# Kernel optimization log

Measured on AMD Instinct MI355X. Metric: run time of the kernel, lower is better.

## Reference

```python
import jax, jax.numpy as jnp
import numpy as np

B, S, H, NH = 2, 2048, 1024, 16
HD = H // NH  # 64
CLIP = 2.5          # clip_init_val; SymQuantizer clamps to [-CLIP, CLIP]
QMAX = 127.0        # 2**(input_bits-1) - 1 for 8-bit symmetric


def sym_quant(x):
    """BiT SymQuantizer, layerwise=True: clamp, layerwise max-abs scale,
    round-to-nearest (scale detached, as in torch .detach())."""
    xc = jnp.clip(x, -CLIP, CLIP)
    m = jax.lax.stop_gradient(jnp.max(jnp.abs(xc)))
    s = QMAX / m
    return jnp.round(xc * s) / s


def setup_inputs() -> dict:
    key = jax.random.key(0)
    ks = jax.random.split(key, 4)
    return {
        "hidden_states": jax.random.normal(ks[0], (B, S, H), jnp.float32),
        "attention_mask": jnp.zeros((B, 1, 1, S), jnp.float32),  # additive mask
        "Wq": jax.random.normal(ks[1], (H, H), jnp.float32) * 0.02,
        "bq": jnp.zeros((H,), jnp.float32),
        "Wk": jax.random.normal(ks[2], (H, H), jnp.float32) * 0.02,
        "bk": jnp.zeros((H,), jnp.float32),
        "Wv": jax.random.normal(ks[3], (H, H), jnp.float32) * 0.02,
        "bv": jnp.zeros((H,), jnp.float32),
        "move_q": jnp.zeros((H,), jnp.float32),
        "move_k": jnp.zeros((H,), jnp.float32),
        "move_v": jnp.zeros((H,), jnp.float32),
    }


def reference(hidden_states, attention_mask, Wq, bq, Wk, bk, Wv, bv,
              move_q, move_k, move_v):
    # QuantizeLinear: quantize input (same quant for all three projections)
    # and quantize weights, then F.linear + bias.
    xq = sym_quant(hidden_states)                       # [B,S,H]
    q = xq @ sym_quant(Wq).T + bq                       # [B,S,H]
    k = xq @ sym_quant(Wk).T + bk
    v = xq @ sym_quant(Wv).T + bv
    # NOTE (bug-faithful): original computes move_q/k/v(mixed_*) but then
    # re-derives query/key/value from mixed_* — LearnableBias has no effect.

    def heads(t):  # [B,S,H] -> [B,NH,S,HD]
        return t.reshape(B, S, NH, HD).transpose(0, 2, 1, 3)

    ql = sym_quant(heads(q))
    kl = sym_quant(heads(k))
    vl = sym_quant(heads(v))

    scores = jnp.einsum('bhqd,bhkd->bhqk', ql, kl) / np.float32(np.sqrt(HD))
    scores = scores + attention_mask                    # [B,NH,S,S]
    probs = jax.nn.softmax(scores, axis=-1)
    # dropout p=0.0 (eval) -> identity; quantize attention probs
    probs = sym_quant(probs)
    ctx = jnp.einsum('bhqk,bhkd->bhqd', probs, vl)      # [B,NH,S,HD]
    ctx = ctx.transpose(0, 2, 1, 3).reshape(B, S, H)
    return ctx, scores
```

## Files before the change

kernel.cpp:

```cpp
#include <hip/hip_runtime.h>
#include <stdint.h>

typedef int i32x4 __attribute__((ext_vector_type(4)));

constexpr int Bb = 2, Ss = 2048, Hh = 1024, NHn = 16;
constexpr int Mm = Bb * Ss;
constexpr int BH = Bb * NHn;
constexpr float CLIPV = 2.5f;

constexpr size_t X8_OFF   = 256;
constexpr size_t W8Q_OFF  = X8_OFF  + (size_t)Mm * Hh;
constexpr size_t W8K_OFF  = W8Q_OFF + (size_t)Hh * Hh;
constexpr size_t W8V_OFF  = W8K_OFF + (size_t)Hh * Hh;
constexpr size_t Q8_OFF   = W8V_OFF + (size_t)Hh * Hh;
constexpr size_t K8_OFF   = Q8_OFF  + (size_t)Mm * Hh;
constexpr size_t V8_OFF   = K8_OFF  + (size_t)Mm * Hh;
constexpr size_t V8T_OFF  = V8_OFF  + (size_t)Mm * Hh;
constexpr size_t RMAX_OFF = V8T_OFF + (size_t)Mm * Hh;
constexpr size_t RSUM_OFF = RMAX_OFF + (size_t)BH * Ss * 4;

__device__ __forceinline__ i32x4 zero4() {
  i32x4 z; z[0] = 0; z[1] = 0; z[2] = 0; z[3] = 0; return z;
}

__global__ void k_init(float* scal) {
  if (threadIdx.x < 7) scal[threadIdx.x] = 0.f;
  if (threadIdx.x == 7) ((unsigned int*)scal)[7] = 0x7f800000u;
}

__global__ __launch_bounds__(256) void k_absmax(
    const float* __restrict__ hs, const float* __restrict__ wq,
    const float* __restrict__ wk, const float* __restrict__ wv,
    float* __restrict__ scal) {
  int b = blockIdx.x;
  const float* src; int sidx, boff;
  if (b < 256)      { src = hs; sidx = 0; boff = b; }
  else if (b < 320) { src = wq; sidx = 1; boff = b - 256; }
  else if (b < 384) { src = wk; sidx = 2; boff = b - 320; }
  else              { src = wv; sidx = 3; boff = b - 384; }
  const float4* p = (const float4*)src + (size_t)boff * 4096 + threadIdx.x;
  float m = 0.f;
#pragma unroll
  for (int i = 0; i < 16; ++i) {
    float4 v = p[i * 256];
    m = fmaxf(m, fmaxf(fmaxf(fabsf(v.x), fabsf(v.y)), fmaxf(fabsf(v.z), fabsf(v.w))));
  }
#pragma unroll
  for (int off = 32; off; off >>= 1) m = fmaxf(m, __shfl_xor(m, off));
  __shared__ float red[4];
  if ((threadIdx.x & 63) == 0) red[threadIdx.x >> 6] = m;
  __syncthreads();
  if (threadIdx.x == 0) {
    m = fmaxf(fmaxf(red[0], red[1]), fmaxf(red[2], red[3]));
    atomicMax((unsigned int*)scal + sidx, __float_as_uint(m));
  }
}

__global__ __launch_bounds__(256) void k_quant_in(
    const float* __restrict__ hs, const float* __restrict__ wq,
    const float* __restrict__ wk, const float* __restrict__ wv,
    const float* __restrict__ scal, char* __restrict__ ws) {
  int b = blockIdx.x;
  const float* src; int sidx, boff; unsigned int* dst;
  if (b < 256)      { src = hs; sidx = 0; boff = b;       dst = (unsigned int*)(ws + X8_OFF); }
  else if (b < 320) { src = wq; sidx = 1; boff = b - 256; dst = (unsigned int*)(ws + W8Q_OFF); }
  else if (b < 384) { src = wk; sidx = 2; boff = b - 320; dst = (unsigned int*)(ws + W8K_OFF); }
  else              { src = wv; sidx = 3; boff = b - 384; dst = (unsigned int*)(ws + W8V_OFF); }
  float s = 127.f / fminf(scal[sidx], CLIPV);
  size_t base = (size_t)boff * 4096 + threadIdx.x;
  const float4* p = (const float4*)src + base;
  dst += base;
#pragma unroll
  for (int i = 0; i < 16; ++i) {
    float4 v = p[i * 256];
    int a0 = __float2int_rn(fminf(fmaxf(v.x, -CLIPV), CLIPV) * s);
    int a1 = __float2int_rn(fminf(fmaxf(v.y, -CLIPV), CLIPV) * s);
    int a2 = __float2int_rn(fminf(fmaxf(v.z, -CLIPV), CLIPV) * s);
    int a3 = __float2int_rn(fminf(fmaxf(v.w, -CLIPV), CLIPV) * s);
    dst[i * 256] = (a0 & 255) | ((a1 & 255) << 8) | ((a2 & 255) << 16) | ((a3 & 255) << 24);
  }
}

__global__ __launch_bounds__(256) void k_qkv_gemm(
    char* __restrict__ ws, float* __restrict__ qkvf,
    const float* __restrict__ bq, const float* __restrict__ bk,
    const float* __restrict__ bv, const float* __restrict__ scal) {
  int wsel = blockIdx.z;
  const char* a8 = ws + X8_OFF;
  const char* b8 = ws + (wsel == 0 ? W8Q_OFF : wsel == 1 ? W8K_OFF : W8V_OFF);
  const float* bias = wsel == 0 ? bq : wsel == 1 ? bk : bv;
  float* outp = qkvf + (size_t)wsel * Mm * Hh;
  float scaleAB = (fminf(scal[0], CLIPV) / 127.f) * (fminf(scal[1 + wsel], CLIPV) / 127.f);

  __shared__ __align__(16) char lA[64][80];
  __shared__ __align__(16) char lB[64][80];
  int t = threadIdx.x;
  int lane = t & 63, w = t >> 6, c = lane & 15, g = lane >> 4;
  int i0 = blockIdx.y * 64;
  int n0 = blockIdx.x * 64;
  int strow = t >> 2, sto = t & 3;
  int stoff = (sto ^ (strow & 3)) * 16;

  i32x4 acc[4];
#pragma unroll
  for (int nt = 0; nt < 4; ++nt) acc[nt] = zero4();

  for (int kc = 0; kc < 16; ++kc) {
    i32x4 va = *(const i32x4*)(a8 + (size_t)(i0 + strow) * 1024 + kc * 64 + sto * 16);
    i32x4 vb = *(const i32x4*)(b8 + (size_t)(n0 + strow) * 1024 + kc * 64 + sto * 16);
    __syncthreads();
    *(i32x4*)&lA[strow][stoff] = va;
    *(i32x4*)&lB[strow][stoff] = vb;
    __syncthreads();
    i32x4 af = *(const i32x4*)&lA[w * 16 + c][(g ^ (c & 3)) * 16];
#pragma unroll
    for (int nt = 0; nt < 4; ++nt) {
      i32x4 bf = *(const i32x4*)&lB[nt * 16 + c][(g ^ (c & 3)) * 16];
      acc[nt] = __builtin_amdgcn_mfma_i32_16x16x64_i8(af, bf, acc[nt], 0, 0, 0);
    }
  }
  float amax = 0.f;
#pragma unroll
  for (int nt = 0; nt < 4; ++nt) {
    int n = n0 + nt * 16 + c;
    float bvv = bias[n];
#pragma unroll
    for (int r = 0; r < 4; ++r) {
      int i = i0 + w * 16 + g * 4 + r;
      float val = fmaf((float)acc[nt][r], scaleAB, bvv);
      outp[(size_t)i * 1024 + n] = val;
      amax = fmaxf(amax, fabsf(val));
    }
  }
#pragma unroll
  for (int off = 32; off; off >>= 1) amax = fmaxf(amax, __shfl_xor(amax, off));
  if (lane == 0) atomicMax((unsigned int*)scal + 4 + wsel, __float_as_uint(amax));
}

__global__ __launch_bounds__(256) void k_quant_qkv(
    char* __restrict__ ws, const float* __restrict__ qkvf,
    const float* __restrict__ scal) {
  int b = blockIdx.x;
  int wsel = b >> 8, boff = b & 255;
  const float* src = qkvf + (size_t)wsel * Mm * Hh;
  unsigned int* dst = (unsigned int*)(ws + (wsel == 0 ? Q8_OFF : wsel == 1 ? K8_OFF : V8_OFF));
  float s = 127.f / fminf(scal[4 + wsel], CLIPV);
  size_t base = (size_t)boff * 4096 + threadIdx.x;
  const float4* p = (const float4*)src + base;
  dst += base;
#pragma unroll
  for (int i = 0; i < 16; ++i) {
    float4 v = p[i * 256];
    int a0 = __float2int_rn(fminf(fmaxf(v.x, -CLIPV), CLIPV) * s);
    int a1 = __float2int_rn(fminf(fmaxf(v.y, -CLIPV), CLIPV) * s);
    int a2 = __float2int_rn(fminf(fmaxf(v.z, -CLIPV), CLIPV) * s);
    int a3 = __float2int_rn(fminf(fmaxf(v.w, -CLIPV), CLIPV) * s);
    dst[i * 256] = (a0 & 255) | ((a1 & 255) << 8) | ((a2 & 255) << 16) | ((a3 & 255) << 24);
  }
}

__global__ __launch_bounds__(256) void k_scores(
    const char* __restrict__ ws, const float* __restrict__ mask,
    float* __restrict__ scores, float* __restrict__ rmax,
    float* __restrict__ rsum, const float* __restrict__ scal) {
  const char* q8 = ws + Q8_OFF;
  const char* k8 = ws + K8_OFF;
  int bh = blockIdx.y, b = bh >> 4;
  int h = bh & 15;
  int i0 = blockIdx.x * 64;
  int t = threadIdx.x, lane = t & 63, w = t >> 6, c = lane & 15, g = lane >> 4;
  float scale8 = (fminf(scal[4], CLIPV) / 127.f) * (fminf(scal[5], CLIPV) / 127.f) * 0.125f;

  __shared__ __align__(16) char lK[128][80];

  int irow = i0 + w * 16 + c;
  i32x4 qf = *(const i32x4*)(q8 + (size_t)(b * 2048 + irow) * 1024 + h * 64 + g * 16);
  const float* maskb = mask + b * 2048;
  float* srow_base = scores + ((size_t)bh * 2048 + irow) * 2048;

  float m = -INFINITY, l = 0.f;
  int strow = t >> 2, sto = t & 3;
  int stoff = (sto ^ (strow & 3)) * 16;

  for (int jc = 0; jc < 2048; jc += 128) {
    i32x4 v0 = *(const i32x4*)(k8 + (size_t)(b * 2048 + jc + strow) * 1024 + h * 64 + sto * 16);
    i32x4 v1 = *(const i32x4*)(k8 + (size_t)(b * 2048 + jc + 64 + strow) * 1024 + h * 64 + sto * 16);
    __syncthreads();
    *(i32x4*)&lK[strow][stoff] = v0;
    *(i32x4*)&lK[64 + strow][stoff] = v1;
    __syncthreads();
#pragma unroll
    for (int jt = 0; jt < 8; ++jt) {
      i32x4 kf = *(const i32x4*)&lK[jt * 16 + c][(g ^ (c & 3)) * 16];
      i32x4 d = __builtin_amdgcn_mfma_i32_16x16x64_i8(kf, qf, zero4(), 0, 0, 0);
      int jbase = jc + jt * 16 + g * 4;
      float4 mv = *(const float4*)(maskb + jbase);
      float s0 = fmaf((float)d[0], scale8, mv.x);
      float s1 = fmaf((float)d[1], scale8, mv.y);
      float s2 = fmaf((float)d[2], scale8, mv.z);
      float s3 = fmaf((float)d[3], scale8, mv.w);
      float tmax = fmaxf(fmaxf(s0, s1), fmaxf(s2, s3));
      float mn = fmaxf(m, tmax);
      l = fmaf(l, __expf(m - mn),
               __expf(s0 - mn) + __expf(s1 - mn) + __expf(s2 - mn) + __expf(s3 - mn));
      m = mn;
      float4 outv; outv.x = s0; outv.y = s1; outv.z = s2; outv.w = s3;
      *(float4*)(srow_base + jbase) = outv;
    }
  }
#pragma unroll
  for (int off = 16; off <= 32; off <<= 1) {
    float mo = __shfl_xor(m, off);
    float lo = __shfl_xor(l, off);
    float mn = fmaxf(m, mo);
    l = l * __expf(m - mn) + lo * __expf(mo - mn);
    m = mn;
  }
  if (g == 0) {
    rmax[(size_t)bh * 2048 + irow] = m;
    rsum[(size_t)bh * 2048 + irow] = l;
  }
  float lmin = l;
#pragma unroll
  for (int off = 1; off <= 8; off <<= 1) lmin = fminf(lmin, __shfl_xor(lmin, off));
  if (lane == 0) atomicMin((unsigned int*)scal + 7, __float_as_uint(lmin));
}

__global__ __launch_bounds__(256) void k_vtrans(char* __restrict__ ws) {
  const char* v8 = ws + V8_OFF;
  char* v8t = ws + V8T_OFF;
  int bh = blockIdx.y, b = bh >> 4, h = bh & 15;
  int jc = blockIdx.x * 64;
  __shared__ __align__(16) char tile[64][80];
  int t = threadIdx.x;
  int j = t >> 2, o = t & 3;
  i32x4 v = *(const i32x4*)(v8 + (size_t)(b * 2048 + jc + j) * 1024 + h * 64 + o * 16);
  *(i32x4*)&tile[j][o * 16] = v;
  __syncthreads();
  int d = t >> 2, seg = t & 3;
  int od[4] = {0, 0, 0, 0};
#pragma unroll
  for (int jj = 0; jj < 16; ++jj)
    od[jj >> 2] |= (int)(unsigned char)tile[seg * 16 + jj][d] << ((jj & 3) * 8);
  i32x4 ov; ov[0] = od[0]; ov[1] = od[1]; ov[2] = od[2]; ov[3] = od[3];
  *(i32x4*)(v8t + ((size_t)bh * 64 + d) * 2048 + jc + seg * 16) = ov;
}

__global__ __launch_bounds__(256) void k_pv(
    char* __restrict__ ws, const float* __restrict__ mask,
    float* __restrict__ ctx, const float* __restrict__ scal) {
  const char* q8 = ws + Q8_OFF;
  const char* k8 = ws + K8_OFF;
  const char* v8t = ws + V8T_OFF;
  const float* rmax = (const float*)(ws + RMAX_OFF);
  const float* rsum = (const float*)(ws + RSUM_OFF);
  int bh = blockIdx.y, b = bh >> 4, h = bh & 15;
  int i0 = blockIdx.x * 64;
  int t = threadIdx.x, lane = t & 63, w = t >> 6, c = lane & 15, g = lane >> 4;
  float scale8 = (fminf(scal[4], CLIPV) / 127.f) * (fminf(scal[5], CLIPV) / 127.f) * 0.125f;
  float min_l = __uint_as_float(((const unsigned int*)scal)[7]);
  float s_p = 127.f * min_l;
  float s_v = 127.f / fminf(scal[6], CLIPV);
  float oscale = 1.f / (s_p * s_v);

  __shared__ __align__(16) char lK[64][80];
  __shared__ __align__(16) int pl[4][16][20];

  int irow = i0 + w * 16 + c;
  i32x4 qf = *(const i32x4*)(q8 + (size_t)(b * 2048 + irow) * 1024 + h * 64 + g * 16);
  float m_i = rmax[(size_t)bh * 2048 + irow];
  float coef = s_p / rsum[(size_t)bh * 2048 + irow];
  const float* maskb = mask + b * 2048;

  i32x4 acc[4];
#pragma unroll
  for (int vt = 0; vt < 4; ++vt) acc[vt] = zero4();

  int strow = t >> 2, sto = t & 3;
  int stoff = (sto ^ (strow & 3)) * 16;

  for (int jc = 0; jc < 2048; jc += 64) {
    i32x4 kv = *(const i32x4*)(k8 + (size_t)(b * 2048 + jc + strow) * 1024 + h * 64 + sto * 16);
    __syncthreads();
    *(i32x4*)&lK[strow][stoff] = kv;
    __syncthreads();
#pragma unroll
    for (int jt = 0; jt < 4; ++jt) {
      i32x4 kf = *(const i32x4*)&lK[jt * 16 + c][(g ^ (c & 3)) * 16];
      i32x4 d = __builtin_amdgcn_mfma_i32_16x16x64_i8(kf, qf, zero4(), 0, 0, 0);
      int jbase = jc + jt * 16 + g * 4;
      float4 mv = *(const float4*)(maskb + jbase);
      float s0 = fmaf((float)d[0], scale8, mv.x);
      float s1 = fmaf((float)d[1], scale8, mv.y);
      float s2 = fmaf((float)d[2], scale8, mv.z);
      float s3 = fmaf((float)d[3], scale8, mv.w);
      int p0 = __float2int_rn(__expf(s0 - m_i) * coef);
      int p1 = __float2int_rn(__expf(s1 - m_i) * coef);
      int p2 = __float2int_rn(__expf(s2 - m_i) * coef);
      int p3 = __float2int_rn(__expf(s3 - m_i) * coef);
      pl[w][c][jt * 4 + g] = (p0 & 255) | ((p1 & 255) << 8) | ((p2 & 255) << 16) | ((p3 & 255) << 24);
    }
    i32x4 pf = *(const i32x4*)&pl[w][c][4 * g];
#pragma unroll
    for (int vt = 0; vt < 4; ++vt) {
      i32x4 vf = *(const i32x4*)(v8t + ((size_t)bh * 64 + vt * 16 + c) * 2048 + jc + g * 16);
      acc[vt] = __builtin_amdgcn_mfma_i32_16x16x64_i8(pf, vf, acc[vt], 0, 0, 0);
    }
  }
#pragma unroll
  for (int vt = 0; vt < 4; ++vt) {
#pragma unroll
    for (int r = 0; r < 4; ++r) {
      int i = i0 + w * 16 + g * 4 + r;
      ctx[(size_t)(b * 2048 + i) * 1024 + h * 64 + vt * 16 + c] = (float)acc[vt][r] * oscale;
    }
  }
}

extern "C" void kernel_launch(void* const* d_in, const int* in_sizes, int n_in,
                              void* d_out, int out_size, void* d_ws, size_t ws_size,
                              hipStream_t stream) {
  const float* hs   = (const float*)d_in[0];
  const float* mask = (const float*)d_in[1];
  const float* Wq   = (const float*)d_in[2];
  const float* bq   = (const float*)d_in[3];
  const float* Wk   = (const float*)d_in[4];
  const float* bk   = (const float*)d_in[5];
  const float* Wv   = (const float*)d_in[6];
  const float* bv   = (const float*)d_in[7];
  char* ws = (char*)d_ws;
  float* scal = (float*)ws;
  float* ctx = (float*)d_out;
  float* scores = (float*)d_out + (size_t)Mm * Hh;
  float* rmax = (float*)(ws + RMAX_OFF);
  float* rsum = (float*)(ws + RSUM_OFF);
  float* qkvf = scores;

  hipLaunchKernelGGL(k_init, dim3(1), dim3(64), 0, stream, scal);
  hipLaunchKernelGGL(k_absmax, dim3(448), dim3(256), 0, stream, hs, Wq, Wk, Wv, scal);
  hipLaunchKernelGGL(k_quant_in, dim3(448), dim3(256), 0, stream, hs, Wq, Wk, Wv, scal, ws);
  hipLaunchKernelGGL(k_qkv_gemm, dim3(16, 64, 3), dim3(256), 0, stream, ws, qkvf, bq, bk, bv, scal);
  hipLaunchKernelGGL(k_quant_qkv, dim3(768), dim3(256), 0, stream, ws, qkvf, scal);
  hipLaunchKernelGGL(k_scores, dim3(32, 32), dim3(256), 0, stream, ws, mask, scores, rmax, rsum, scal);
  hipLaunchKernelGGL(k_vtrans, dim3(32, 32), dim3(256), 0, stream, ws);
  hipLaunchKernelGGL(k_pv, dim3(32, 32), dim3(256), 0, stream, ws, mask, ctx, scal);
}
```

Before: 983.5 us.

## Coalesce score and output stores via LDS staging, swapped MFMA operands, block swizzle

Swaps the MFMA A/B operands in the QKV GEMM and PV kernels so each lane holds four consecutive columns, which allows float4 stores of outputs and bias loads. The scores kernel stages each 16x64 tile in padded LDS and writes full contiguous row segments with nontemporal stores, replacing scattered 16-byte stores into a 16 MB score matrix. Scores and PV now launch on a 1D grid with an XCD-aware swizzle so blocks sharing a head land on the same die. The cost is extra LDS traffic and shared memory per block in the scores kernel.

```diff
diff --git a/kernel.cpp b/kernel.cpp
--- a/kernel.cpp
+++ b/kernel.cpp
@@ -2,6 +2,7 @@
 #include <stdint.h>
 
 typedef int i32x4 __attribute__((ext_vector_type(4)));
+typedef float f32x4 __attribute__((ext_vector_type(4)));
 
 constexpr int Bb = 2, Ss = 2048, Hh = 1024, NHn = 16;
 constexpr int Mm = Bb * Ss;
@@ -116,21 +117,22 @@
 #pragma unroll
     for (int nt = 0; nt < 4; ++nt) {
       i32x4 bf = *(const i32x4*)&lB[nt * 16 + c][(g ^ (c & 3)) * 16];
-      acc[nt] = __builtin_amdgcn_mfma_i32_16x16x64_i8(af, bf, acc[nt], 0, 0, 0);
+      acc[nt] = __builtin_amdgcn_mfma_i32_16x16x64_i8(bf, af, acc[nt], 0, 0, 0);
     }
   }
+  int i = i0 + w * 16 + c;
   float amax = 0.f;
 #pragma unroll
   for (int nt = 0; nt < 4; ++nt) {
-    int n = n0 + nt * 16 + c;
-    float bvv = bias[n];
-#pragma unroll
-    for (int r = 0; r < 4; ++r) {
-      int i = i0 + w * 16 + g * 4 + r;
-      float val = fmaf((float)acc[nt][r], scaleAB, bvv);
-      outp[(size_t)i * 1024 + n] = val;
-      amax = fmaxf(amax, fabsf(val));
-    }
+    int n = n0 + nt * 16 + g * 4;
+    float4 bv4 = *(const float4*)(bias + n);
+    float4 o;
+    o.x = fmaf((float)acc[nt][0], scaleAB, bv4.x);
+    o.y = fmaf((float)acc[nt][1], scaleAB, bv4.y);
+    o.z = fmaf((float)acc[nt][2], scaleAB, bv4.z);
+    o.w = fmaf((float)acc[nt][3], scaleAB, bv4.w);
+    *(float4*)(outp + (size_t)i * 1024 + n) = o;
+    amax = fmaxf(amax, fmaxf(fmaxf(fabsf(o.x), fabsf(o.y)), fmaxf(fabsf(o.z), fabsf(o.w))));
   }
 #pragma unroll
   for (int off = 32; off; off >>= 1) amax = fmaxf(amax, __shfl_xor(amax, off));
@@ -165,18 +167,21 @@
     float* __restrict__ rsum, const float* __restrict__ scal) {
   const char* q8 = ws + Q8_OFF;
   const char* k8 = ws + K8_OFF;
-  int bh = blockIdx.y, b = bh >> 4;
-  int h = bh & 15;
-  int i0 = blockIdx.x * 64;
+  int lin = blockIdx.x;
+  int swz = (lin & 7) * 128 + (lin >> 3);
+  int bh = swz >> 5, iblk = swz & 31;
+  int b = bh >> 4, h = bh & 15;
+  int i0 = iblk * 64;
   int t = threadIdx.x, lane = t & 63, w = t >> 6, c = lane & 15, g = lane >> 4;
   float scale8 = (fminf(scal[4], CLIPV) / 127.f) * (fminf(scal[5], CLIPV) / 127.f) * 0.125f;
 
   __shared__ __align__(16) char lK[128][80];
+  __shared__ __align__(16) float sbuf[4][16][69];
 
   int irow = i0 + w * 16 + c;
   i32x4 qf = *(const i32x4*)(q8 + (size_t)(b * 2048 + irow) * 1024 + h * 64 + g * 16);
   const float* maskb = mask + b * 2048;
-  float* srow_base = scores + ((size_t)bh * 2048 + irow) * 2048;
+  float* srow0 = scores + ((size_t)bh * 2048 + i0 + w * 16) * 2048;
 
   float m = -INFINITY, l = 0.f;
   int strow = t >> 2, sto = t & 3;
@@ -190,22 +195,34 @@
     *(i32x4*)&lK[64 + strow][stoff] = v1;
     __syncthreads();
 #pragma unroll
-    for (int jt = 0; jt < 8; ++jt) {
-      i32x4 kf = *(const i32x4*)&lK[jt * 16 + c][(g ^ (c & 3)) * 16];
-      i32x4 d = __builtin_amdgcn_mfma_i32_16x16x64_i8(kf, qf, zero4(), 0, 0, 0);
-      int jbase = jc + jt * 16 + g * 4;
-      float4 mv = *(const float4*)(maskb + jbase);
-      float s0 = fmaf((float)d[0], scale8, mv.x);
-      float s1 = fmaf((float)d[1], scale8, mv.y);
-      float s2 = fmaf((float)d[2], scale8, mv.z);
-      float s3 = fmaf((float)d[3], scale8, mv.w);
-      float tmax = fmaxf(fmaxf(s0, s1), fmaxf(s2, s3));
-      float mn = fmaxf(m, tmax);
-      l = fmaf(l, __expf(m - mn),
-               __expf(s0 - mn) + __expf(s1 - mn) + __expf(s2 - mn) + __expf(s3 - mn));
-      m = mn;
-      float4 outv; outv.x = s0; outv.y = s1; outv.z = s2; outv.w = s3;
-      *(float4*)(srow_base + jbase) = outv;
+    for (int jg = 0; jg < 2; ++jg) {
+#pragma unroll
+      for (int jtm = 0; jtm < 4; ++jtm) {
+        int jt = jg * 4 + jtm;
+        i32x4 kf = *(const i32x4*)&lK[jt * 16 + c][(g ^ (c & 3)) * 16];
+        i32x4 d = __builtin_amdgcn_mfma_i32_16x16x64_i8(kf, qf, zero4(), 0, 0, 0);
+        int jbase = jc + jt * 16 + g * 4;
+        float4 mv = *(const float4*)(maskb + jbase);
+        float s0 = fmaf((float)d[0], scale8, mv.x);
+        float s1 = fmaf((float)d[1], scale8, mv.y);
+        float s2 = fmaf((float)d[2], scale8, mv.z);
+        float s3 = fmaf((float)d[3], scale8, mv.w);
+        float tmax = fmaxf(fmaxf(s0, s1), fmaxf(s2, s3));
+        float mn = fmaxf(m, tmax);
+        l = fmaf(l, __expf(m - mn),
+                 __expf(s0 - mn) + __expf(s1 - mn) + __expf(s2 - mn) + __expf(s3 - mn));
+        m = mn;
+        float* sp = &sbuf[w][c][jtm * 16 + g * 4];
+        sp[0] = s0; sp[1] = s1; sp[2] = s2; sp[3] = s3;
+      }
+      int h4 = lane >> 4, k2 = (lane & 15) * 4;
+#pragma unroll
+      for (int rr = 0; rr < 4; ++rr) {
+        int row = rr * 4 + h4;
+        f32x4 val = *(const f32x4*)&sbuf[w][row][k2];
+        __builtin_nontemporal_store(val,
+            (f32x4*)(srow0 + (size_t)row * 2048 + jc + jg * 64 + k2));
+      }
     }
   }
 #pragma unroll
@@ -254,8 +271,11 @@
   const char* v8t = ws + V8T_OFF;
   const float* rmax = (const float*)(ws + RMAX_OFF);
   const float* rsum = (const float*)(ws + RSUM_OFF);
-  int bh = blockIdx.y, b = bh >> 4, h = bh & 15;
-  int i0 = blockIdx.x * 64;
+  int lin = blockIdx.x;
+  int swz = (lin & 7) * 128 + (lin >> 3);
+  int bh = swz >> 5, iblk = swz & 31;
+  int b = bh >> 4, h = bh & 15;
+  int i0 = iblk * 64;
   int t = threadIdx.x, lane = t & 63, w = t >> 6, c = lane & 15, g = lane >> 4;
   float scale8 = (fminf(scal[4], CLIPV) / 127.f) * (fminf(scal[5], CLIPV) / 127.f) * 0.125f;
   float min_l = __uint_as_float(((const unsigned int*)scal)[7]);
@@ -304,16 +324,19 @@
 #pragma unroll
     for (int vt = 0; vt < 4; ++vt) {
       i32x4 vf = *(const i32x4*)(v8t + ((size_t)bh * 64 + vt * 16 + c) * 2048 + jc + g * 16);
-      acc[vt] = __builtin_amdgcn_mfma_i32_16x16x64_i8(pf, vf, acc[vt], 0, 0, 0);
+      acc[vt] = __builtin_amdgcn_mfma_i32_16x16x64_i8(vf, pf, acc[vt], 0, 0, 0);
     }
   }
+  int i = i0 + w * 16 + c;
 #pragma unroll
   for (int vt = 0; vt < 4; ++vt) {
-#pragma unroll
-    for (int r = 0; r < 4; ++r) {
-      int i = i0 + w * 16 + g * 4 + r;
-      ctx[(size_t)(b * 2048 + i) * 1024 + h * 64 + vt * 16 + c] = (float)acc[vt][r] * oscale;
-    }
+    f32x4 o;
+    o[0] = (float)acc[vt][0] * oscale;
+    o[1] = (float)acc[vt][1] * oscale;
+    o[2] = (float)acc[vt][2] * oscale;
+    o[3] = (float)acc[vt][3] * oscale;
+    __builtin_nontemporal_store(o,
+        (f32x4*)(ctx + (size_t)(b * 2048 + i) * 1024 + h * 64 + vt * 16 + g * 4));
   }
 }
 
@@ -341,7 +364,7 @@
   hipLaunchKernelGGL(k_quant_in, dim3(448), dim3(256), 0, stream, hs, Wq, Wk, Wv, scal, ws);
   hipLaunchKernelGGL(k_qkv_gemm, dim3(16, 64, 3), dim3(256), 0, stream, ws, qkvf, bq, bk, bv, scal);
   hipLaunchKernelGGL(k_quant_qkv, dim3(768), dim3(256), 0, stream, ws, qkvf, scal);
-  hipLaunchKernelGGL(k_scores, dim3(32, 32), dim3(256), 0, stream, ws, mask, scores, rmax, rsum, scal);
+  hipLaunchKernelGGL(k_scores, dim3(1024), dim3(256), 0, stream, ws, mask, scores, rmax, rsum, scal);
   hipLaunchKernelGGL(k_vtrans, dim3(32, 32), dim3(256), 0, stream, ws);
-  hipLaunchKernelGGL(k_pv, dim3(32, 32), dim3(256), 0, stream, ws, mask, ctx, scal);
-}
+  hipLaunchKernelGGL(k_pv, dim3(1024), dim3(256), 0, stream, ws, mask, ctx, scal);
+}
```

Measured after the change: 917.6 us. -6.7%, faster.
